# Kernel tuning notes

Hardware: AMD Instinct MI355X
Metric: run time of the kernel (lower is better)

Reference implementation:

```python
import jax, jax.numpy as jnp
import numpy as np

D_IN = 4096
D_OUT = 4096
RANK = 16
NUM_EXPERTS = 8
TOP_K = 2
SCALING = 32.0 / RANK  # lora_alpha / r = 2.0


def setup_inputs() -> dict:
    key = jax.random.key(0)
    ks = jax.random.split(key, 6)
    x = jax.random.normal(ks[0], (4, 2048, D_IN), dtype=jnp.float32)
    W_base = jax.random.normal(ks[1], (D_OUT, D_IN), dtype=jnp.float32) * (1.0 / np.sqrt(D_IN))
    b_base = jax.random.normal(ks[2], (D_OUT,), dtype=jnp.float32) * 0.01
    W_router = jax.random.normal(ks[3], (NUM_EXPERTS, D_IN), dtype=jnp.float32) * 0.01
    # kaiming-uniform-like A; B nonzero (module inits B to zero, but zero B makes outputs/grads trivial)
    A_stack = jax.random.uniform(ks[4], (NUM_EXPERTS, RANK, D_IN), dtype=jnp.float32,
                                 minval=-1.0, maxval=1.0) * (1.0 / np.sqrt(D_IN))
    B_stack = jax.random.normal(ks[5], (NUM_EXPERTS, D_OUT, RANK), dtype=jnp.float32) * 0.02
    return {"x": x, "W_base": W_base, "b_base": b_base,
            "W_router": W_router, "A_stack": A_stack, "B_stack": B_stack}


def reference(x, W_base, b_base, W_router, A_stack, B_stack):
    orig_shape = x.shape
    xf = x.reshape(-1, D_IN)                                # [N, d_in]
    # Router: softmax -> top-k -> renormalize
    logits = xf @ W_router.T                                # [N, E]
    probs = jax.nn.softmax(logits, axis=-1)
    topk_p, topk_i = jax.lax.top_k(probs, TOP_K)            # [N, K]
    topk_p = topk_p / jnp.sum(topk_p, axis=-1, keepdims=True)
    # Combine weights per expert (scatter top-k probs into [N, E])
    combine = jnp.sum(jax.nn.one_hot(topk_i, NUM_EXPERTS, dtype=xf.dtype)
                      * topk_p[..., None], axis=1)          # [N, E]
    # Low-rank expert path: x @ A_e^T, weight, then @ B_e^T, summed over experts
    h = jnp.einsum('nd,erd->ner', xf, A_stack)              # [N, E, r]
    h = h * combine[..., None]
    lora_out = jnp.einsum('ner,eor->no', h, B_stack) * SCALING  # [N, d_out]
    base_out = xf @ W_base.T + b_base                       # [N, d_out]
    out = base_out + lora_out
    return out.reshape(orig_shape[:-1] + (D_OUT,))
```

## Files before the change

### kernel.cpp

```cpp
#include <hip/hip_runtime.h>

#define D_IN   4096
#define D_OUT  4096
#define N_TOK  8192
#define RANK   16
#define NEXP   8
#define ER     128
#define KCAT   4224
#define SCALING 2.0f

typedef __attribute__((ext_vector_type(8))) short short8;
typedef __attribute__((ext_vector_type(4))) float f32x4;
typedef __attribute__((ext_vector_type(4))) unsigned short us4;
typedef unsigned int uint;

__device__ __forceinline__ unsigned short f2bf(float f) {
  unsigned u = __float_as_uint(f);
  u += 0x7FFFu + ((u >> 16) & 1u);
  return (unsigned short)(u >> 16);
}

__device__ __forceinline__ void gload_lds16(const void* g, void* l) {
  __builtin_amdgcn_global_load_lds(
      (const __attribute__((address_space(1))) unsigned int*)g,
      (__attribute__((address_space(3))) unsigned int*)l, 16, 0, 0);
}

__global__ void prep_kernel(const float* __restrict__ W, const float* __restrict__ A,
                            const float* __restrict__ B,
                            unsigned short* __restrict__ Wcat,
                            unsigned short* __restrict__ Ab) {
  const int NW4 = (D_OUT * D_IN) / 4;
  const int NA4 = (ER * D_IN) / 4;
  const int NB4 = (D_OUT * ER) / 4;
  const int total = NW4 + NA4 + NB4;
  for (int i = blockIdx.x * blockDim.x + threadIdx.x; i < total;
       i += gridDim.x * blockDim.x) {
    if (i < NW4) {
      float4 v = ((const float4*)W)[i];
      us4 o = { f2bf(v.x), f2bf(v.y), f2bf(v.z), f2bf(v.w) };
      int row = i >> 10, kq = i & 1023;
      ((us4*)(Wcat + (size_t)row * KCAT))[kq] = o;
    } else if (i < NW4 + NA4) {
      int j = i - NW4;
      float4 v = ((const float4*)A)[j];
      us4 o = { f2bf(v.x), f2bf(v.y), f2bf(v.z), f2bf(v.w) };
      ((us4*)Ab)[j] = o;
    } else {
      int j = i - NW4 - NA4;
      int o = j >> 5; int rem = j & 31; int e = rem >> 2; int rq = rem & 3;
      float4 v = *(const float4*)(B + (size_t)e * D_OUT * RANK + o * RANK + rq * 4);
      us4 ob = { f2bf(v.x), f2bf(v.y), f2bf(v.z), f2bf(v.w) };
      *(us4*)(Wcat + (size_t)o * KCAT + D_IN + e * 16 + rq * 4) = ob;
    }
  }
}

__global__ __launch_bounds__(256) void router_kernel(
    const float* __restrict__ X, const float* __restrict__ Wr,
    unsigned short* __restrict__ Xcat, float* __restrict__ Comb) {
  int wave = threadIdx.x >> 6, lane = threadIdx.x & 63;
  int tok0 = blockIdx.x * 16 + wave * 4;
  float acc[4][8];
#pragma unroll
  for (int t = 0; t < 4; ++t)
#pragma unroll
    for (int e = 0; e < 8; ++e) acc[t][e] = 0.f;
  const float4* X4 = (const float4*)X;
  const float4* W4 = (const float4*)Wr;
#pragma unroll 1
  for (int it = 0; it < 16; ++it) {
    int kq = it * 64 + lane;
    float4 w[8];
#pragma unroll
    for (int e = 0; e < 8; ++e) w[e] = W4[e * 1024 + kq];
#pragma unroll
    for (int t = 0; t < 4; ++t) {
      float4 xv = X4[(size_t)(tok0 + t) * 1024 + kq];
      us4 xb = { f2bf(xv.x), f2bf(xv.y), f2bf(xv.z), f2bf(xv.w) };
      ((us4*)(Xcat + (size_t)(tok0 + t) * KCAT))[kq] = xb;
#pragma unroll
      for (int e = 0; e < 8; ++e)
        acc[t][e] = fmaf(xv.x, w[e].x, fmaf(xv.y, w[e].y,
                     fmaf(xv.z, w[e].z, fmaf(xv.w, w[e].w, acc[t][e]))));
    }
  }
#pragma unroll
  for (int t = 0; t < 4; ++t)
#pragma unroll
    for (int e = 0; e < 8; ++e) {
      float v = acc[t][e];
      for (int off = 32; off; off >>= 1) v += __shfl_xor(v, off, 64);
      acc[t][e] = v;
    }
#pragma unroll
  for (int t = 0; t < 4; ++t) {
    float m1 = acc[t][0]; int i1 = 0;
#pragma unroll
    for (int e = 1; e < 8; ++e) if (acc[t][e] > m1) { m1 = acc[t][e]; i1 = e; }
    float m2 = -1e30f; int i2 = 0;
#pragma unroll
    for (int e = 0; e < 8; ++e)
      if (e != i1 && acc[t][e] > m2) { m2 = acc[t][e]; i2 = e; }
    float w1 = 1.f / (1.f + expf(m2 - m1));
    if (lane < 8) {
      float v = (lane == i1) ? w1 : (lane == i2) ? (1.f - w1) : 0.f;
      Comb[(size_t)(tok0 + t) * 8 + lane] = v * SCALING;
    }
  }
}

#define HSTG(S) { const uint hbase = (S) * 40960u; \
  _Pragma("unroll") for (int c = 0; c < 2; ++c) { gload_lds16(pa[c], ldsc + hbase + da[c]); pa[c] += 128; } \
  _Pragma("unroll") for (int c = 0; c < 8; ++c) { gload_lds16(pb[c], ldsc + hbase + db[c]); pb[c] += 128; } }

#define HTILE(S, S2, DOSTG, VM) { const uint hb = (S) * 40960u; \
  short8 af[4]; short8 bfr[4][4]; \
  _Pragma("unroll") for (int kk = 0; kk < 4; ++kk) af[kk] = *(const short8*)(ldsc + hb + oA[kk]); \
  _Pragma("unroll") for (int n = 0; n < 4; ++n) \
    _Pragma("unroll") for (int kk = 0; kk < 4; ++kk) bfr[n][kk] = *(const short8*)(ldsc + hb + oB[n][kk]); \
  if (DOSTG) HSTG(S2); \
  __builtin_amdgcn_sched_barrier(0); __builtin_amdgcn_s_barrier(); __builtin_amdgcn_sched_barrier(0); \
  __builtin_amdgcn_s_setprio(1); \
  _Pragma("unroll") for (int kk = 0; kk < 4; ++kk) \
    _Pragma("unroll") for (int n = 0; n < 4; ++n) \
      acc[n] = __builtin_amdgcn_mfma_f32_16x16x32_bf16(af[kk], bfr[n][kk], acc[n], 0, 0, 0); \
  __builtin_amdgcn_s_setprio(0); \
  __builtin_amdgcn_sched_barrier(0); \
  asm volatile("s_waitcnt vmcnt(" #VM ")" ::: ); \
  __builtin_amdgcn_s_barrier(); __builtin_amdgcn_sched_barrier(0); }

__global__ __launch_bounds__(256, 1) void h_gemm_kernel(
    unsigned short* Xcat, const unsigned short* __restrict__ Ab,
    const float* __restrict__ Comb) {
  __shared__ unsigned short hlds[61440];
  char* ldsc = (char*)hlds;
  const int tid = threadIdx.x, wave = tid >> 6, lane = tid & 63;
  const int wm = wave >> 1, wn = wave & 1;
  const int row0 = blockIdx.x * 32;

  const unsigned short* pa[2]; uint da[2];
#pragma unroll
  for (int c = 0; c < 2; ++c) {
    int ch = c * 256 + tid, row = ch >> 4, s = ch & 15;
    pa[c] = Xcat + (size_t)(row0 + row) * KCAT + (s ^ ((row >> 1) & 7)) * 8;
    da[c] = (uint)ch * 16;
  }
  const unsigned short* pb[8]; uint db[8];
#pragma unroll
  for (int c = 0; c < 8; ++c) {
    int ch = c * 256 + tid, row = ch >> 4, s = ch & 15;
    pb[c] = Ab + (size_t)row * D_IN + (s ^ ((row >> 1) & 7)) * 8;
    db[c] = 8192u + (uint)ch * 16;
  }

  uint oA[4], oB[4][4];
  {
    int rA = wm * 16 + (lane & 15);
#pragma unroll
    for (int kk = 0; kk < 4; ++kk) {
      int slot = kk * 4 + (lane >> 4);
      oA[kk] = (uint)rA * 256 + (uint)((slot ^ ((rA >> 1) & 7)) * 16);
    }
#pragma unroll
    for (int n = 0; n < 4; ++n) {
      int rB = wn * 64 + n * 16 + (lane & 15);
#pragma unroll
      for (int kk = 0; kk < 4; ++kk) {
        int slot = kk * 4 + (lane >> 4);
        oB[n][kk] = 8192u + (uint)rB * 256 + (uint)((slot ^ ((rB >> 1) & 7)) * 16);
      }
    }
  }

  f32x4 acc[4];
#pragma unroll
  for (int n = 0; n < 4; ++n) acc[n] = (f32x4){0.f, 0.f, 0.f, 0.f};

  HSTG(0); HSTG(1);
  asm volatile("s_waitcnt vmcnt(10)" ::: );
  __builtin_amdgcn_s_barrier();
  __builtin_amdgcn_sched_barrier(0);

#pragma unroll 1
  for (int i3 = 0; i3 < 10; ++i3) {
    HTILE(0, 2, 1, 10);
    HTILE(1, 0, 1, 10);
    HTILE(2, 1, 1, 10);
  }
  HTILE(0, 0, 0, 0);
  HTILE(1, 0, 0, 0);

#pragma unroll
  for (int n = 0; n < 4; ++n) {
    int c = wn * 64 + n * 16 + (lane & 15);
    int e = c >> 4;
#pragma unroll
    for (int i = 0; i < 4; ++i) {
      int r = row0 + wm * 16 + (lane >> 4) * 4 + i;
      float v = acc[n][i] * Comb[(size_t)r * 8 + e];
      Xcat[(size_t)r * KCAT + D_IN + c] = f2bf(v);
    }
  }
}

#define STG_A(S) { gload_lds16(pA0, ldsc + (S) * 32768u + dA0); pA0 += 32; \
                   gload_lds16(pA1, ldsc + (S) * 32768u + dA1); pA1 += 32; }
#define STG_B(S) { gload_lds16(pB0, ldsc + (S) * 32768u + dB0); pB0 += 32; \
                   gload_lds16(pB1, ldsc + (S) * 32768u + dB1); pB1 += 32; }

#define MTILE(SLOT, SLOT3, DOSTG, VM) { \
  const uint sb = (SLOT) * 32768u; \
  short8 a0[4], bf[4], a1[4]; \
  _Pragma("unroll") for (int m = 0; m < 4; ++m) a0[m] = *(const short8*)(ldsc + sb + offA[m]); \
  _Pragma("unroll") for (int n = 0; n < 4; ++n) bf[n] = *(const short8*)(ldsc + sb + offB[n]); \
  __builtin_amdgcn_sched_barrier(0); \
  _Pragma("unroll") for (int m = 0; m < 4; ++m) a1[m] = *(const short8*)(ldsc + sb + offA[4 + m]); \
  if (DOSTG) { STG_A(SLOT3); STG_B(SLOT3); } \
  __builtin_amdgcn_sched_barrier(0); \
  __builtin_amdgcn_s_barrier(); \
  __builtin_amdgcn_sched_barrier(0); \
  asm volatile("s_waitcnt lgkmcnt(4)" ::: ); \
  __builtin_amdgcn_sched_barrier(0); \
  __builtin_amdgcn_s_setprio(1); \
  _Pragma("unroll") for (int m = 0; m < 4; ++m) \
    _Pragma("unroll") for (int n = 0; n < 4; ++n) \
      acc[m][n] = __builtin_amdgcn_mfma_f32_16x16x32_bf16(a0[m], bf[n], acc[m][n], 0, 0, 0); \
  __builtin_amdgcn_sched_barrier(0); \
  asm volatile("s_waitcnt lgkmcnt(0)" ::: ); \
  __builtin_amdgcn_sched_barrier(0); \
  _Pragma("unroll") for (int m = 0; m < 4; ++m) \
    _Pragma("unroll") for (int n = 0; n < 4; ++n) \
      acc[4 + m][n] = __builtin_amdgcn_mfma_f32_16x16x32_bf16(a1[m], bf[n], acc[4 + m][n], 0, 0, 0); \
  __builtin_amdgcn_s_setprio(0); \
  __builtin_amdgcn_sched_barrier(0); \
  asm volatile("s_waitcnt vmcnt(" #VM ")" ::: ); \
  __builtin_amdgcn_s_barrier(); \
  __builtin_amdgcn_sched_barrier(0); }

__global__ __launch_bounds__(512, 2) void main_gemm_kernel(
    const unsigned short* __restrict__ Xcat, const unsigned short* __restrict__ Wcat,
    const float* __restrict__ bias, float* __restrict__ Out) {
  __shared__ unsigned short lds[4 * 16384];
  char* ldsc = (char*)lds;
  const int tid = threadIdx.x;
  const int wave = tid >> 6, lane = tid & 63;
  const int wm = wave >> 2, wn = wave & 3;
  const int ks = lane >> 4;

  int bid = blockIdx.x;
  int swz = (bid & 7) * 64 + (bid >> 3);
  int mb = swz >> 4, nb = swz & 15;
  const int row0 = mb * 256, col0 = nb * 256;

  const unsigned short *pA0, *pA1, *pB0, *pB1;
  uint dA0, dA1, dB0, dB1;
  {
    int ch0 = tid, ch1 = 512 + tid;
    int rr0 = ch0 >> 2, ss0 = (ch0 & 3) ^ ((ch0 >> 3) & 3);
    int rr1 = ch1 >> 2, ss1 = (ch1 & 3) ^ ((ch1 >> 3) & 3);
    pA0 = Xcat + (size_t)(row0 + rr0) * KCAT + ss0 * 8;
    pA1 = Xcat + (size_t)(row0 + rr1) * KCAT + ss1 * 8;
    pB0 = Wcat + (size_t)(col0 + rr0) * KCAT + ss0 * 8;
    pB1 = Wcat + (size_t)(col0 + rr1) * KCAT + ss1 * 8;
    dA0 = (uint)wave * 1024;          dA1 = 8192u + (uint)wave * 1024;
    dB0 = 16384u + (uint)wave * 1024; dB1 = 24576u + (uint)wave * 1024;
  }

  uint offA[8], offB[4];
#pragma unroll
  for (int mi = 0; mi < 8; ++mi) {
    int r = wm * 128 + mi * 16 + (lane & 15);
    offA[mi] = (uint)r * 64 + (uint)((ks ^ ((r >> 1) & 3)) * 16);
  }
#pragma unroll
  for (int ni = 0; ni < 4; ++ni) {
    int r = wn * 64 + ni * 16 + (lane & 15);
    offB[ni] = 16384u + (uint)r * 64 + (uint)((ks ^ ((r >> 1) & 3)) * 16);
  }

  f32x4 acc[8][4];
#pragma unroll
  for (int mi = 0; mi < 8; ++mi)
#pragma unroll
    for (int ni = 0; ni < 4; ++ni) acc[mi][ni] = (f32x4){0.f, 0.f, 0.f, 0.f};

  STG_A(0); STG_B(0); STG_A(1); STG_B(1); STG_A(2); STG_B(2);
  asm volatile("s_waitcnt vmcnt(8)" ::: );
  __builtin_amdgcn_s_barrier();
  __builtin_amdgcn_sched_barrier(0);

#pragma unroll 1
  for (int i4 = 0; i4 < 32; ++i4) {
    MTILE(0, 3, 1, 8);
    MTILE(1, 0, 1, 8);
    MTILE(2, 1, 1, 8);
    MTILE(3, 2, 1, 8);
  }
  MTILE(0, 3, 1, 8);
  MTILE(1, 0, 0, 4);
  MTILE(2, 0, 0, 0);
  MTILE(3, 0, 0, 0);

#pragma unroll
  for (int ni = 0; ni < 4; ++ni) {
    const int c = col0 + wn * 64 + ni * 16 + (lane & 15);
    const float bv = bias[c];
#pragma unroll
    for (int mi = 0; mi < 8; ++mi) {
#pragma unroll
      for (int i = 0; i < 4; ++i) {
        int r = row0 + wm * 128 + mi * 16 + ks * 4 + i;
        Out[(size_t)r * D_OUT + c] = acc[mi][ni][i] + bv;
      }
    }
  }
}

extern "C" void kernel_launch(void* const* d_in, const int* in_sizes, int n_in,
                              void* d_out, int out_size, void* d_ws, size_t ws_size,
                              hipStream_t stream) {
  const float* x        = (const float*)d_in[0];
  const float* W_base   = (const float*)d_in[1];
  const float* b_base   = (const float*)d_in[2];
  const float* W_router = (const float*)d_in[3];
  const float* A_stack  = (const float*)d_in[4];
  const float* B_stack  = (const float*)d_in[5];
  float* out = (float*)d_out;

  char* ws = (char*)d_ws;
  unsigned short* Xcat = (unsigned short*)(ws);
  unsigned short* Wcat = (unsigned short*)(ws + 69206016);
  unsigned short* Ab   = (unsigned short*)(ws + 103809024);
  float*          Comb = (float*)(ws + 104857600);

  hipLaunchKernelGGL(prep_kernel, dim3(2048), dim3(256), 0, stream,
                     W_base, A_stack, B_stack, Wcat, Ab);
  hipLaunchKernelGGL(router_kernel, dim3(512), dim3(256), 0, stream,
                     x, W_router, Xcat, Comb);
  hipLaunchKernelGGL(h_gemm_kernel, dim3(256), dim3(256), 0, stream,
                     Xcat, Ab, Comb);
  hipLaunchKernelGGL(main_gemm_kernel, dim3(512), dim3(512), 0, stream,
                     Xcat, Wcat, b_base, out);
}
```

Before: 348.8 us.

## Fuse prep and router kernels and split GEMM staging around barriers

Merges the weight-conversion prep kernel and the router kernel into one launch, using block-index ranges so both run concurrently and one launch is saved. In the main GEMM tile loop, the A and B global-to-LDS stages are now issued in separate phases between extra barriers, and the explicit lgkmcnt waits are removed. This aims to spread memory traffic across the MFMA phases. It adds two more workgroup barriers per tile, and correctness of the LDS reads now relies on the barriers rather than explicit waits.

```diff
diff --git a/kernel.cpp b/kernel.cpp
--- a/kernel.cpp
+++ b/kernel.cpp
@@ -26,86 +26,87 @@
       (__attribute__((address_space(3))) unsigned int*)l, 16, 0, 0);
 }
 
-__global__ void prep_kernel(const float* __restrict__ W, const float* __restrict__ A,
-                            const float* __restrict__ B,
-                            unsigned short* __restrict__ Wcat,
-                            unsigned short* __restrict__ Ab) {
-  const int NW4 = (D_OUT * D_IN) / 4;
-  const int NA4 = (ER * D_IN) / 4;
-  const int NB4 = (D_OUT * ER) / 4;
-  const int total = NW4 + NA4 + NB4;
-  for (int i = blockIdx.x * blockDim.x + threadIdx.x; i < total;
-       i += gridDim.x * blockDim.x) {
-    if (i < NW4) {
-      float4 v = ((const float4*)W)[i];
-      us4 o = { f2bf(v.x), f2bf(v.y), f2bf(v.z), f2bf(v.w) };
-      int row = i >> 10, kq = i & 1023;
-      ((us4*)(Wcat + (size_t)row * KCAT))[kq] = o;
-    } else if (i < NW4 + NA4) {
-      int j = i - NW4;
-      float4 v = ((const float4*)A)[j];
-      us4 o = { f2bf(v.x), f2bf(v.y), f2bf(v.z), f2bf(v.w) };
-      ((us4*)Ab)[j] = o;
-    } else {
-      int j = i - NW4 - NA4;
-      int o = j >> 5; int rem = j & 31; int e = rem >> 2; int rq = rem & 3;
-      float4 v = *(const float4*)(B + (size_t)e * D_OUT * RANK + o * RANK + rq * 4);
-      us4 ob = { f2bf(v.x), f2bf(v.y), f2bf(v.z), f2bf(v.w) };
-      *(us4*)(Wcat + (size_t)o * KCAT + D_IN + e * 16 + rq * 4) = ob;
-    }
-  }
-}
-
-__global__ __launch_bounds__(256) void router_kernel(
+__global__ __launch_bounds__(256) void fused_prep_router_kernel(
     const float* __restrict__ X, const float* __restrict__ Wr,
-    unsigned short* __restrict__ Xcat, float* __restrict__ Comb) {
-  int wave = threadIdx.x >> 6, lane = threadIdx.x & 63;
-  int tok0 = blockIdx.x * 16 + wave * 4;
-  float acc[4][8];
-#pragma unroll
-  for (int t = 0; t < 4; ++t)
-#pragma unroll
-    for (int e = 0; e < 8; ++e) acc[t][e] = 0.f;
-  const float4* X4 = (const float4*)X;
-  const float4* W4 = (const float4*)Wr;
+    const float* __restrict__ W, const float* __restrict__ A,
+    const float* __restrict__ B,
+    unsigned short* __restrict__ Xcat, float* __restrict__ Comb,
+    unsigned short* __restrict__ Wcat, unsigned short* __restrict__ Ab) {
+  if (blockIdx.x < 512) {
+    int wave = threadIdx.x >> 6, lane = threadIdx.x & 63;
+    int tok0 = blockIdx.x * 16 + wave * 4;
+    float acc[4][8];
+#pragma unroll
+    for (int t = 0; t < 4; ++t)
+#pragma unroll
+      for (int e = 0; e < 8; ++e) acc[t][e] = 0.f;
+    const float4* X4 = (const float4*)X;
+    const float4* W4 = (const float4*)Wr;
 #pragma unroll 1
-  for (int it = 0; it < 16; ++it) {
-    int kq = it * 64 + lane;
-    float4 w[8];
-#pragma unroll
-    for (int e = 0; e < 8; ++e) w[e] = W4[e * 1024 + kq];
+    for (int it = 0; it < 16; ++it) {
+      int kq = it * 64 + lane;
+      float4 w[8];
+#pragma unroll
+      for (int e = 0; e < 8; ++e) w[e] = W4[e * 1024 + kq];
+#pragma unroll
+      for (int t = 0; t < 4; ++t) {
+        float4 xv = X4[(size_t)(tok0 + t) * 1024 + kq];
+        us4 xb = { f2bf(xv.x), f2bf(xv.y), f2bf(xv.z), f2bf(xv.w) };
+        ((us4*)(Xcat + (size_t)(tok0 + t) * KCAT))[kq] = xb;
+#pragma unroll
+        for (int e = 0; e < 8; ++e)
+          acc[t][e] = fmaf(xv.x, w[e].x, fmaf(xv.y, w[e].y,
+                       fmaf(xv.z, w[e].z, fmaf(xv.w, w[e].w, acc[t][e]))));
+      }
+    }
+#pragma unroll
+    for (int t = 0; t < 4; ++t)
+#pragma unroll
+      for (int e = 0; e < 8; ++e) {
+        float v = acc[t][e];
+        for (int off = 32; off; off >>= 1) v += __shfl_xor(v, off, 64);
+        acc[t][e] = v;
+      }
 #pragma unroll
     for (int t = 0; t < 4; ++t) {
-      float4 xv = X4[(size_t)(tok0 + t) * 1024 + kq];
-      us4 xb = { f2bf(xv.x), f2bf(xv.y), f2bf(xv.z), f2bf(xv.w) };
-      ((us4*)(Xcat + (size_t)(tok0 + t) * KCAT))[kq] = xb;
+      float m1 = acc[t][0]; int i1 = 0;
+#pragma unroll
+      for (int e = 1; e < 8; ++e) if (acc[t][e] > m1) { m1 = acc[t][e]; i1 = e; }
+      float m2 = -1e30f; int i2 = 0;
 #pragma unroll
       for (int e = 0; e < 8; ++e)
-        acc[t][e] = fmaf(xv.x, w[e].x, fmaf(xv.y, w[e].y,
-                     fmaf(xv.z, w[e].z, fmaf(xv.w, w[e].w, acc[t][e]))));
-    }
-  }
-#pragma unroll
-  for (int t = 0; t < 4; ++t)
-#pragma unroll
-    for (int e = 0; e < 8; ++e) {
-      float v = acc[t][e];
-      for (int off = 32; off; off >>= 1) v += __shfl_xor(v, off, 64);
-      acc[t][e] = v;
-    }
-#pragma unroll
-  for (int t = 0; t < 4; ++t) {
-    float m1 = acc[t][0]; int i1 = 0;
-#pragma unroll
-    for (int e = 1; e < 8; ++e) if (acc[t][e] > m1) { m1 = acc[t][e]; i1 = e; }
-    float m2 = -1e30f; int i2 = 0;
-#pragma unroll
-    for (int e = 0; e < 8; ++e)
-      if (e != i1 && acc[t][e] > m2) { m2 = acc[t][e]; i2 = e; }
-    float w1 = 1.f / (1.f + expf(m2 - m1));
-    if (lane < 8) {
-      float v = (lane == i1) ? w1 : (lane == i2) ? (1.f - w1) : 0.f;
-      Comb[(size_t)(tok0 + t) * 8 + lane] = v * SCALING;
+        if (e != i1 && acc[t][e] > m2) { m2 = acc[t][e]; i2 = e; }
+      float w1 = 1.f / (1.f + expf(m2 - m1));
+      if (lane < 8) {
+        float v = (lane == i1) ? w1 : (lane == i2) ? (1.f - w1) : 0.f;
+        Comb[(size_t)(tok0 + t) * 8 + lane] = v * SCALING;
+      }
+    }
+  } else {
+    const int NW4 = (D_OUT * D_IN) / 4;
+    const int NA4 = (ER * D_IN) / 4;
+    const int NB4 = (D_OUT * ER) / 4;
+    const int total = NW4 + NA4 + NB4;
+    const int stride = 2048 * 256;
+    for (int i = (blockIdx.x - 512) * blockDim.x + threadIdx.x; i < total;
+         i += stride) {
+      if (i < NW4) {
+        float4 v = ((const float4*)W)[i];
+        us4 o = { f2bf(v.x), f2bf(v.y), f2bf(v.z), f2bf(v.w) };
+        int row = i >> 10, kq = i & 1023;
+        ((us4*)(Wcat + (size_t)row * KCAT))[kq] = o;
+      } else if (i < NW4 + NA4) {
+        int j = i - NW4;
+        float4 v = ((const float4*)A)[j];
+        us4 o = { f2bf(v.x), f2bf(v.y), f2bf(v.z), f2bf(v.w) };
+        ((us4*)Ab)[j] = o;
+      } else {
+        int j = i - NW4 - NA4;
+        int o = j >> 5; int rem = j & 31; int e = rem >> 2; int rq = rem & 3;
+        float4 v = *(const float4*)(B + (size_t)e * D_OUT * RANK + o * RANK + rq * 4);
+        us4 ob = { f2bf(v.x), f2bf(v.y), f2bf(v.z), f2bf(v.w) };
+        *(us4*)(Wcat + (size_t)o * KCAT + D_IN + e * 16 + rq * 4) = ob;
+      }
     }
   }
 }
@@ -214,21 +215,24 @@
   short8 a0[4], bf[4], a1[4]; \
   _Pragma("unroll") for (int m = 0; m < 4; ++m) a0[m] = *(const short8*)(ldsc + sb + offA[m]); \
   _Pragma("unroll") for (int n = 0; n < 4; ++n) bf[n] = *(const short8*)(ldsc + sb + offB[n]); \
-  __builtin_amdgcn_sched_barrier(0); \
   _Pragma("unroll") for (int m = 0; m < 4; ++m) a1[m] = *(const short8*)(ldsc + sb + offA[4 + m]); \
-  if (DOSTG) { STG_A(SLOT3); STG_B(SLOT3); } \
+  if (DOSTG) STG_A(SLOT3); \
   __builtin_amdgcn_sched_barrier(0); \
   __builtin_amdgcn_s_barrier(); \
-  __builtin_amdgcn_sched_barrier(0); \
-  asm volatile("s_waitcnt lgkmcnt(4)" ::: ); \
   __builtin_amdgcn_sched_barrier(0); \
   __builtin_amdgcn_s_setprio(1); \
   _Pragma("unroll") for (int m = 0; m < 4; ++m) \
     _Pragma("unroll") for (int n = 0; n < 4; ++n) \
       acc[m][n] = __builtin_amdgcn_mfma_f32_16x16x32_bf16(a0[m], bf[n], acc[m][n], 0, 0, 0); \
-  __builtin_amdgcn_sched_barrier(0); \
-  asm volatile("s_waitcnt lgkmcnt(0)" ::: ); \
-  __builtin_amdgcn_sched_barrier(0); \
+  __builtin_amdgcn_s_setprio(0); \
+  __builtin_amdgcn_sched_barrier(0); \
+  __builtin_amdgcn_s_barrier(); \
+  __builtin_amdgcn_sched_barrier(0); \
+  if (DOSTG) STG_B(SLOT3); \
+  __builtin_amdgcn_sched_barrier(0); \
+  __builtin_amdgcn_s_barrier(); \
+  __builtin_amdgcn_sched_barrier(0); \
+  __builtin_amdgcn_s_setprio(1); \
   _Pragma("unroll") for (int m = 0; m < 4; ++m) \
     _Pragma("unroll") for (int n = 0; n < 4; ++n) \
       acc[4 + m][n] = __builtin_amdgcn_mfma_f32_16x16x32_bf16(a1[m], bf[n], acc[4 + m][n], 0, 0, 0); \
@@ -334,10 +338,8 @@
   unsigned short* Ab   = (unsigned short*)(ws + 103809024);
   float*          Comb = (float*)(ws + 104857600);
 
-  hipLaunchKernelGGL(prep_kernel, dim3(2048), dim3(256), 0, stream,
-                     W_base, A_stack, B_stack, Wcat, Ab);
-  hipLaunchKernelGGL(router_kernel, dim3(512), dim3(256), 0, stream,
-                     x, W_router, Xcat, Comb);
+  hipLaunchKernelGGL(fused_prep_router_kernel, dim3(2560), dim3(256), 0, stream,
+                     x, W_router, W_base, A_stack, B_stack, Xcat, Comb, Wcat, Ab);
   hipLaunchKernelGGL(h_gemm_kernel, dim3(256), dim3(256), 0, stream,
                      Xcat, Ab, Comb);
   hipLaunchKernelGGL(main_gemm_kernel, dim3(512), dim3(512), 0, stream,
```

Result: faster. 341.3 us (-2.1%).
